# Performance work log

Hardware: AMD Instinct MI355X
Metric: run time of the kernel (lower is better)

Reference implementation:

```python
import jax, jax.numpy as jnp
import numpy as np

# Model dims: H features, N half-state-size, R low-rank, CH output channels, KL kernel length
H, N, R, CH, KL = 512, 64, 1, 1, 4096


def setup_inputs() -> dict:
    key = jax.random.key(0)
    ks = jax.random.split(key, 8)
    log_dt = jax.random.uniform(ks[0], (H,), minval=float(np.log(1e-3)), maxval=float(np.log(1e-1)), dtype=jnp.float32)
    # Hurwitz-like poles: negative real part, HiPPO-like imaginary ladder
    w_re = -0.5 - jax.random.uniform(ks[1], (H, N), dtype=jnp.float32)
    w_im = jnp.broadcast_to(np.float32(np.pi) * jnp.arange(N, dtype=jnp.float32), (H, N))
    B_re = jax.random.normal(ks[2], (1, H, N), dtype=jnp.float32)
    B_im = jax.random.normal(ks[3], (1, H, N), dtype=jnp.float32)
    # small low-rank correction keeps the Woodbury denominator away from zero
    P_re = 0.1 * jax.random.normal(ks[4], (R, H, N), dtype=jnp.float32)
    P_im = 0.1 * jax.random.normal(ks[5], (R, H, N), dtype=jnp.float32)
    C_re = jax.random.normal(ks[6], (CH, H, N), dtype=jnp.float32)
    C_im = jax.random.normal(ks[7], (CH, H, N), dtype=jnp.float32)
    return dict(log_dt=log_dt, w_re=w_re, w_im=w_im, B_re=B_re, B_im=B_im,
                P_re=P_re, P_im=P_im, C_re=C_re, C_im=C_im, L=KL)


def _kernel(log_dt, w_re, w_im, B_re, B_im, P_re, P_im, C_re, C_im, L):
    dt = jnp.exp(log_dt)                                   # (H,)
    w = (w_re + 1j * w_im) * dt[:, None]                   # (H,N) discretized poles w*dt
    B = B_re + 1j * B_im                                   # (1,H,N)
    P = P_re + 1j * P_im                                   # (R,H,N)
    Q = jnp.conj(P)                                        # hurwitz=False path: Q = conj(P)
    C = C_re + 1j * C_im                                   # (CH,H,N)

    Lf = L // 2 + 1
    kk = jnp.arange(Lf)
    omega = jnp.exp((-2j * np.pi) * kk / L)                # FFT roots of unity (complex64)
    den = 1.0 + omega
    # Nyquist node (omega = -1) handled analytically below; guard the division
    safe_den = jnp.where(jnp.abs(den) < 1e-6, jnp.ones_like(den), den)
    z = 2.0 * (1.0 - omega) / safe_den                     # bilinear-transform nodes

    Bc = jnp.concatenate([B, P], axis=0)                   # (1+R,H,N)
    Cc = jnp.concatenate([C, Q], axis=0)                   # (CH+R,H,N)
    v = Bc[:, None] * Cc[None]                             # (1+R,CH+R,H,N)

    # Cauchy kernel: r[a,b,h,l] = sum_n v[a,b,h,n] / (z[l] - w[h,n])
    recip = 1.0 / (z[None, None, :] - w[:, :, None])       # (H,N,Lf)
    r = jnp.einsum('abhn,hnl->abhl', v, recip)             # (1+R,CH+R,H,Lf)
    r = r * dt[None, None, :, None]

    # rank-1 Woodbury correction
    k_f = r[:-1, :-1] - r[:-1, -1:] * r[-1:, :-1] / (1.0 + r[-1:, -1:])
    k_f = k_f * 2.0 / safe_den

    if L % 2 == 0:
        # analytic z -> inf limit at the Nyquist node: dt/2 * sum_n v00
        nyq = 0.5 * dt[None, None, :] * jnp.sum(v[:-1, :-1], axis=-1)  # (1,CH,H)
        k_f = k_f.at[..., -1].set(nyq)

    k = jnp.fft.irfft(k_f, n=L, axis=-1)[..., :L]          # (1,CH,H,L) real
    return k[-1]                                           # (CH,H,L)


def reference(log_dt, w_re, w_im, B_re, B_im, P_re, P_im, C_re, C_im, L):
    return _kernel(log_dt, w_re, w_im, B_re, B_im, P_re, P_im, C_re, C_im, L)
```

## Files before the change

### kernel.cpp

```cpp
#include <hip/hip_runtime.h>
#include <hip/hip_bf16.h>
#include <math.h>


#define HH   512
#define NN   64
#define LLEN 4096
#define MM   2048
#define NTHREADS 512
#define ZPAD(i) ((i) + ((i) >> 4))

typedef float v2f __attribute__((ext_vector_type(2)));

__device__ __forceinline__ float sinr(float r) { return __builtin_amdgcn_sinf(r); }
__device__ __forceinline__ float cosr(float r) { return __builtin_amdgcn_cosf(r); }
__device__ __forceinline__ float rcpf(float x) { return __builtin_amdgcn_rcpf(x); }

__device__ __forceinline__ void cauchy_step(
    const v2f tv, const v2f mwi, const v2f nr, const v2f wr2,
    const v2f v00r, const v2f v00i, const v2f v01r, const v2f v01i,
    const v2f v10r, const v2f v10i, const v2f v11,
    v2f& a00r, v2f& a00i, v2f& a01r, v2f& a01i,
    v2f& a10r, v2f& a10i, v2f& a11r, v2f& a11i)
{
    const v2f dim = __builtin_elementwise_fma(tv, (v2f){2.0f, 2.0f}, mwi);
    const v2f den = __builtin_elementwise_fma(dim, dim, wr2);
    const float ip = rcpf(den.x * den.y);
    v2f inv; inv.x = den.y * ip; inv.y = den.x * ip;
    const v2f ur = nr * inv;
    const v2f ui = -(dim * inv);
    a00r = __builtin_elementwise_fma( v00r, ur, a00r);
    a00r = __builtin_elementwise_fma(-v00i, ui, a00r);
    a00i = __builtin_elementwise_fma( v00r, ui, a00i);
    a00i = __builtin_elementwise_fma( v00i, ur, a00i);
    a01r = __builtin_elementwise_fma( v01r, ur, a01r);
    a01r = __builtin_elementwise_fma(-v01i, ui, a01r);
    a01i = __builtin_elementwise_fma( v01r, ui, a01i);
    a01i = __builtin_elementwise_fma( v01i, ur, a01i);
    a10r = __builtin_elementwise_fma( v10r, ur, a10r);
    a10r = __builtin_elementwise_fma(-v10i, ui, a10r);
    a10i = __builtin_elementwise_fma( v10r, ui, a10i);
    a10i = __builtin_elementwise_fma( v10i, ur, a10i);
    a11r = __builtin_elementwise_fma( v11,  ur, a11r);
    a11i = __builtin_elementwise_fma( v11,  ui, a11i);
}

__device__ __forceinline__ void woodbury_K(
    const v2f tv,
    const v2f a00r, const v2f a00i, const v2f a01r, const v2f a01i,
    const v2f a10r, const v2f a10i, const v2f a11r, const v2f a11i,
    v2f& Kr, v2f& Ki)
{
    const v2f dr = a11r + 1.0f;
    const v2f di = a11i;
    const v2f dd = __builtin_elementwise_fma(dr, dr, di * di);
    v2f dinv; dinv.x = rcpf(dd.x); dinv.y = rcpf(dd.y);
    const v2f numr = a01r * a10r - a01i * a10i;
    const v2f numi = a01r * a10i + a01i * a10r;
    const v2f cr = (numr * dr + numi * di) * dinv;
    const v2f ci = (numi * dr - numr * di) * dinv;
    const v2f Wr = a00r - cr;
    const v2f Wi = a00i - ci;
    Kr = __builtin_elementwise_fma(-tv, Wi, Wr);
    Ki = __builtin_elementwise_fma( tv, Wr, Wi);
}

__global__ __launch_bounds__(NTHREADS, 4) void ssknplr_kernel(
    const float* __restrict__ log_dt,
    const float* __restrict__ w_re, const float* __restrict__ w_im,
    const float* __restrict__ B_re, const float* __restrict__ B_im,
    const float* __restrict__ P_re, const float* __restrict__ P_im,
    const float* __restrict__ C_re, const float* __restrict__ C_im,
    float* __restrict__ out)
{
    __shared__ float4 s_q0[NN];
    __shared__ float4 s_q1[NN];
    __shared__ float2 s_q2[NN];
    __shared__ float2 s_Z[ZPAD(MM) + 1];

    const int h   = blockIdx.x;
    const int tid = threadIdx.x;

    if (tid < NN) {
        const int n   = tid;
        const int idx = h * NN + n;
        const float dt = expf(log_dt[h]);
        const float wr = w_re[idx] * dt;
        const float wi = w_im[idx] * dt;
        const float Br = B_re[idx], Bi = B_im[idx];
        const float Pr = P_re[idx], Pi = P_im[idx];
        const float Cr = C_re[idx], Ci = C_im[idx];
        const float v00r = dt * (Br * Cr - Bi * Ci);
        const float v00i = dt * (Br * Ci + Bi * Cr);
        const float v01r = dt * (Br * Pr + Bi * Pi);
        const float v01i = dt * (Bi * Pr - Br * Pi);
        const float v10r = dt * (Pr * Cr - Pi * Ci);
        const float v10i = dt * (Pr * Ci + Pi * Cr);
        const float v11  = dt * (Pr * Pr + Pi * Pi);
        s_q0[n] = make_float4(-wi, -wr, wr * wr, v00r);
        s_q1[n] = make_float4(v00i, v01r, v01i, v10r);
        s_q2[n] = make_float2(v10i, v11);
    }
    __syncthreads();

    v2f tvA, tvB;
    {
        const float rA = (float)tid         * (1.0f / 8192.0f);
        const float rB = (float)(tid + 512) * (1.0f / 8192.0f);
        const float sA = sinr(rA), cA = cosr(rA);
        const float sB = sinr(rB), cB = cosr(rB);
        tvA.x = sA * rcpf(cA);
        tvA.y = (tid == 0) ? 1.0f : cA * rcpf(sA);
        tvB.x = sB * rcpf(cB);
        tvB.y = cB * rcpf(sB);
    }

    v2f A00r = {0.f,0.f}, A00i = {0.f,0.f}, A01r = {0.f,0.f}, A01i = {0.f,0.f};
    v2f A10r = {0.f,0.f}, A10i = {0.f,0.f}, A11r = {0.f,0.f}, A11i = {0.f,0.f};
    v2f B00r = {0.f,0.f}, B00i = {0.f,0.f}, B01r = {0.f,0.f}, B01i = {0.f,0.f};
    v2f B10r = {0.f,0.f}, B10i = {0.f,0.f}, B11r = {0.f,0.f}, B11i = {0.f,0.f};

    #pragma unroll 4
    for (int n = 0; n < NN; ++n) {
        const float4 q0 = s_q0[n];
        const float4 q1 = s_q1[n];
        const float2 q2 = s_q2[n];
        const v2f mwi  = {q0.x, q0.x}, nr   = {q0.y, q0.y}, wr2 = {q0.z, q0.z};
        const v2f v00r = {q0.w, q0.w}, v00i = {q1.x, q1.x};
        const v2f v01r = {q1.y, q1.y}, v01i = {q1.z, q1.z};
        const v2f v10r = {q1.w, q1.w}, v10i = {q2.x, q2.x};
        const v2f v11  = {q2.y, q2.y};
        cauchy_step(tvA, mwi, nr, wr2, v00r, v00i, v01r, v01i, v10r, v10i, v11,
                    A00r, A00i, A01r, A01i, A10r, A10i, A11r, A11i);
        cauchy_step(tvB, mwi, nr, wr2, v00r, v00i, v01r, v01i, v10r, v10i, v11,
                    B00r, B00i, B01r, B01i, B10r, B10i, B11r, B11i);
    }

    {
        v2f Kr, Ki;
        woodbury_K(tvA, A00r, A00i, A01r, A01i, A10r, A10i, A11r, A11i, Kr, Ki);
        if (tid == 0) {
            float sr = 0.f;
            for (int n = 0; n < NN; ++n) sr += s_q0[n].w;
            const float KN = 0.5f * sr;
            s_Z[ZPAD(0)]    = make_float2(0.5f * (Kr.x + KN), 0.5f * (Kr.x - KN));
            s_Z[ZPAD(1024)] = make_float2(Kr.y, -Ki.y);
        } else {
            const int k = tid, Mk = MM - tid;
            const float rk = (float)k * (1.0f / 4096.0f);
            const float sk = sinr(rk), ck = cosr(rk);
            const float Pr = 0.5f * (Kr.x + Kr.y), Pi = 0.5f * (Ki.x - Ki.y);
            const float Dr = 0.5f * (Kr.x - Kr.y), Di = 0.5f * (Ki.x + Ki.y);
            const float al = sk * Dr + ck * Di;
            const float be = ck * Dr - sk * Di;
            s_Z[ZPAD(k)]  = make_float2(Pr - al, Pi + be);
            s_Z[ZPAD(Mk)] = make_float2(Pr + al, be - Pi);
        }
    }
    {
        v2f Kr, Ki;
        woodbury_K(tvB, B00r, B00i, B01r, B01i, B10r, B10i, B11r, B11i, Kr, Ki);
        const int k = 512 + tid, Mk = 1536 - tid;
        const float rk = (float)k * (1.0f / 4096.0f);
        const float sk = sinr(rk), ck = cosr(rk);
        const float Pr = 0.5f * (Kr.x + Kr.y), Pi = 0.5f * (Ki.x - Ki.y);
        const float Dr = 0.5f * (Kr.x - Kr.y), Di = 0.5f * (Ki.x + Ki.y);
        const float al = sk * Dr + ck * Di;
        const float be = ck * Dr - sk * Di;
        s_Z[ZPAD(k)]  = make_float2(Pr - al, Pi + be);
        s_Z[ZPAD(Mk)] = make_float2(Pr + al, be - Pi);
    }
    __syncthreads();

    for (int s = 10; s >= 1; s -= 2) {
        const int H = 1 << s;
        const int Q = H >> 1;
        const float scale = rcpf((float)(2 * H));
        {
            const int b    = tid;
            const int j    = b & (Q - 1);
            const int base = ((b >> (s - 1)) << (s + 1)) + j;
            const int i0 = base, i1 = base + Q, i2 = base + H, i3 = base + H + Q;
            const float rev = (float)j * scale;
            const float c  = cosr(rev);
            const float sn = sinr(rev);
            const float wbr = c * c - sn * sn;
            const float wbi = 2.0f * c * sn;
            const float2 u0 = s_Z[ZPAD(i0)];
            const float2 u1 = s_Z[ZPAD(i1)];
            const float2 u2 = s_Z[ZPAD(i2)];
            const float2 u3 = s_Z[ZPAD(i3)];
            const float a0r = u0.x + u2.x, a0i = u0.y + u2.y;
            const float d0r = u0.x - u2.x, d0i = u0.y - u2.y;
            const float a1r = u1.x + u3.x, a1i = u1.y + u3.y;
            const float d1r = u1.x - u3.x, d1i = u1.y - u3.y;
            const float e0r = d0r * c  - d0i * sn, e0i = d0r * sn + d0i * c;
            const float e1r = -(d1r * sn) - d1i * c, e1i = d1r * c - d1i * sn;
            s_Z[ZPAD(i0)] = make_float2(a0r + a1r, a0i + a1i);
            const float t0r = a0r - a1r, t0i = a0i - a1i;
            s_Z[ZPAD(i1)] = make_float2(t0r * wbr - t0i * wbi, t0r * wbi + t0i * wbr);
            s_Z[ZPAD(i2)] = make_float2(e0r + e1r, e0i + e1i);
            const float t1r = e0r - e1r, t1i = e0i - e1i;
            s_Z[ZPAD(i3)] = make_float2(t1r * wbr - t1i * wbi, t1r * wbi + t1i * wbr);
        }
        __syncthreads();
    }

    {
        const float scale = 1.0f / (float)MM;
        const int r0 = (int)(__brev((unsigned)tid) >> 21);
        const int zb = ZPAD(r0);
        const float2 z0 = s_Z[zb + 0];
        const float2 z1 = s_Z[zb + 1];
        const float2 z2 = s_Z[zb + 2];
        const float2 z3 = s_Z[zb + 3];
        float2* o2 = (float2*)out + (size_t)h * MM;
        o2[tid]        = make_float2((z0.x + z1.x) * scale, (z0.y + z1.y) * scale);
        o2[tid + 512]  = make_float2((z2.x + z3.x) * scale, (z2.y + z3.y) * scale);
        o2[tid + 1024] = make_float2((z0.x - z1.x) * scale, (z0.y - z1.y) * scale);
        o2[tid + 1536] = make_float2((z2.x - z3.x) * scale, (z2.y - z3.y) * scale);
    }
}

extern "C" void kernel_launch(void* const* d_in, const int* in_sizes, int n_in,
                              void* d_out, int out_size, void* d_ws, size_t ws_size,
                              hipStream_t stream) {
    const float* log_dt = (const float*)d_in[0];
    const float* w_re   = (const float*)d_in[1];
    const float* w_im   = (const float*)d_in[2];
    const float* B_re   = (const float*)d_in[3];
    const float* B_im   = (const float*)d_in[4];
    const float* P_re   = (const float*)d_in[5];
    const float* P_im   = (const float*)d_in[6];
    const float* C_re   = (const float*)d_in[7];
    const float* C_im   = (const float*)d_in[8];
    float* out = (float*)d_out;

    ssknplr_kernel<<<dim3(HH), dim3(NTHREADS), 0, stream>>>(
        log_dt, w_re, w_im, B_re, B_im, P_re, P_im, C_re, C_im, out);
}
```

Before: 35.05 us.

## Halve block size, four Cauchy points per thread, radix-8 inverse FFT

The block shrinks from 512 to 256 threads, and each thread now evaluates four pairs of Cauchy frequency nodes instead of two. The five radix-4 FFT passes, each followed by a barrier, are replaced by three radix-8 passes and a final pair of radix-4 butterflies. The shared-memory padding formula changes to reduce bank conflicts for the new strides. This cuts barrier count and shared-memory round trips. In exchange it raises per-thread register pressure (32 v2f accumulators) and lowers launch_bounds occupancy to 2.

```diff
diff --git a/kernel.cpp b/kernel.cpp
--- a/kernel.cpp
+++ b/kernel.cpp
@@ -7,8 +7,8 @@
 #define NN   64
 #define LLEN 4096
 #define MM   2048
-#define NTHREADS 512
-#define ZPAD(i) ((i) + ((i) >> 4))
+#define NTHREADS 256
+#define ZP(i) ((i) + ((i) >> 4) + ((i) >> 8))
 
 typedef float v2f __attribute__((ext_vector_type(2)));
 
@@ -65,7 +65,57 @@
     Ki = __builtin_elementwise_fma( tv, Wr, Wi);
 }
 
-__global__ __launch_bounds__(NTHREADS, 4) void ssknplr_kernel(
+__device__ __forceinline__ void radix8(float xr[8], float xi[8], const float rev)
+{
+    const float c   = cosr(rev), s = sinr(rev);
+    const float w2r = c * c - s * s, w2i = 2.0f * c * s;
+    const float w4r = w2r * w2r - w2i * w2i;
+    const float w4i = 2.0f * w2r * w2i;
+    const float RH  = 0.70710678118654752440f;
+    const float cms = RH * (c - s), cps = RH * (c + s);
+
+    const float Ar0 = xr[0] + xr[4], Ai0 = xi[0] + xi[4];
+    const float Ar1 = xr[1] + xr[5], Ai1 = xi[1] + xi[5];
+    const float Ar2 = xr[2] + xr[6], Ai2 = xi[2] + xi[6];
+    const float Ar3 = xr[3] + xr[7], Ai3 = xi[3] + xi[7];
+    float dr, di;
+    dr = xr[0] - xr[4]; di = xi[0] - xi[4];
+    const float Br0 = dr * c - di * s,      Bi0 = dr * s + di * c;
+    dr = xr[1] - xr[5]; di = xi[1] - xi[5];
+    const float Br1 = dr * cms - di * cps,  Bi1 = dr * cps + di * cms;
+    dr = xr[2] - xr[6]; di = xi[2] - xi[6];
+    const float Br2 = -dr * s - di * c,     Bi2 = dr * c - di * s;
+    dr = xr[3] - xr[7]; di = xi[3] - xi[7];
+    const float Br3 = -dr * cps - di * cms, Bi3 = dr * cms - di * cps;
+
+    const float Cr0 = Ar0 + Ar2, Ci0 = Ai0 + Ai2;
+    const float Cr1 = Ar1 + Ar3, Ci1 = Ai1 + Ai3;
+    dr = Ar0 - Ar2; di = Ai0 - Ai2;
+    const float Dr0 = dr * w2r - di * w2i,  Di0 = dr * w2i + di * w2r;
+    dr = Ar1 - Ar3; di = Ai1 - Ai3;
+    const float Dr1 = -dr * w2i - di * w2r, Di1 = dr * w2r - di * w2i;
+    const float Er0 = Br0 + Br2, Ei0 = Bi0 + Bi2;
+    const float Er1 = Br1 + Br3, Ei1 = Bi1 + Bi3;
+    dr = Br0 - Br2; di = Bi0 - Bi2;
+    const float Fr0 = dr * w2r - di * w2i,  Fi0 = dr * w2i + di * w2r;
+    dr = Br1 - Br3; di = Bi1 - Bi3;
+    const float Fr1 = -dr * w2i - di * w2r, Fi1 = dr * w2r - di * w2i;
+
+    xr[0] = Cr0 + Cr1; xi[0] = Ci0 + Ci1;
+    dr = Cr0 - Cr1; di = Ci0 - Ci1;
+    xr[1] = dr * w4r - di * w4i; xi[1] = dr * w4i + di * w4r;
+    xr[2] = Dr0 + Dr1; xi[2] = Di0 + Di1;
+    dr = Dr0 - Dr1; di = Di0 - Di1;
+    xr[3] = dr * w4r - di * w4i; xi[3] = dr * w4i + di * w4r;
+    xr[4] = Er0 + Er1; xi[4] = Ei0 + Ei1;
+    dr = Er0 - Er1; di = Ei0 - Ei1;
+    xr[5] = dr * w4r - di * w4i; xi[5] = dr * w4i + di * w4r;
+    xr[6] = Fr0 + Fr1; xi[6] = Fi0 + Fi1;
+    dr = Fr0 - Fr1; di = Fi0 - Fi1;
+    xr[7] = dr * w4r - di * w4i; xi[7] = dr * w4i + di * w4r;
+}
+
+__global__ __launch_bounds__(NTHREADS, 2) void ssknplr_kernel(
     const float* __restrict__ log_dt,
     const float* __restrict__ w_re, const float* __restrict__ w_im,
     const float* __restrict__ B_re, const float* __restrict__ B_im,
@@ -76,7 +126,7 @@
     __shared__ float4 s_q0[NN];
     __shared__ float4 s_q1[NN];
     __shared__ float2 s_q2[NN];
-    __shared__ float2 s_Z[ZPAD(MM) + 1];
+    __shared__ float2 s_Z[ZP(MM - 1) + 1];
 
     const int h   = blockIdx.x;
     const int tid = threadIdx.x;
@@ -103,24 +153,33 @@
     }
     __syncthreads();
 
-    v2f tvA, tvB;
+    v2f tvA, tvB, tvC, tvD;
     {
         const float rA = (float)tid         * (1.0f / 8192.0f);
-        const float rB = (float)(tid + 512) * (1.0f / 8192.0f);
+        const float rB = (float)(tid + 256) * (1.0f / 8192.0f);
+        const float rC = (float)(tid + 512) * (1.0f / 8192.0f);
+        const float rD = (float)(tid + 768) * (1.0f / 8192.0f);
         const float sA = sinr(rA), cA = cosr(rA);
         const float sB = sinr(rB), cB = cosr(rB);
+        const float sC = sinr(rC), cC = cosr(rC);
+        const float sD = sinr(rD), cD = cosr(rD);
         tvA.x = sA * rcpf(cA);
         tvA.y = (tid == 0) ? 1.0f : cA * rcpf(sA);
-        tvB.x = sB * rcpf(cB);
-        tvB.y = cB * rcpf(sB);
-    }
-
-    v2f A00r = {0.f,0.f}, A00i = {0.f,0.f}, A01r = {0.f,0.f}, A01i = {0.f,0.f};
-    v2f A10r = {0.f,0.f}, A10i = {0.f,0.f}, A11r = {0.f,0.f}, A11i = {0.f,0.f};
-    v2f B00r = {0.f,0.f}, B00i = {0.f,0.f}, B01r = {0.f,0.f}, B01i = {0.f,0.f};
-    v2f B10r = {0.f,0.f}, B10i = {0.f,0.f}, B11r = {0.f,0.f}, B11i = {0.f,0.f};
-
-    #pragma unroll 4
+        tvB.x = sB * rcpf(cB);  tvB.y = cB * rcpf(sB);
+        tvC.x = sC * rcpf(cC);  tvC.y = cC * rcpf(sC);
+        tvD.x = sD * rcpf(cD);  tvD.y = cD * rcpf(sD);
+    }
+
+    v2f A00r={0.f,0.f},A00i={0.f,0.f},A01r={0.f,0.f},A01i={0.f,0.f};
+    v2f A10r={0.f,0.f},A10i={0.f,0.f},A11r={0.f,0.f},A11i={0.f,0.f};
+    v2f B00r={0.f,0.f},B00i={0.f,0.f},B01r={0.f,0.f},B01i={0.f,0.f};
+    v2f B10r={0.f,0.f},B10i={0.f,0.f},B11r={0.f,0.f},B11i={0.f,0.f};
+    v2f C00r={0.f,0.f},C00i={0.f,0.f},C01r={0.f,0.f},C01i={0.f,0.f};
+    v2f C10r={0.f,0.f},C10i={0.f,0.f},C11r={0.f,0.f},C11i={0.f,0.f};
+    v2f D00r={0.f,0.f},D00i={0.f,0.f},D01r={0.f,0.f},D01i={0.f,0.f};
+    v2f D10r={0.f,0.f},D10i={0.f,0.f},D11r={0.f,0.f},D11i={0.f,0.f};
+
+    #pragma unroll 2
     for (int n = 0; n < NN; ++n) {
         const float4 q0 = s_q0[n];
         const float4 q1 = s_q1[n];
@@ -134,6 +193,10 @@
                     A00r, A00i, A01r, A01i, A10r, A10i, A11r, A11i);
         cauchy_step(tvB, mwi, nr, wr2, v00r, v00i, v01r, v01i, v10r, v10i, v11,
                     B00r, B00i, B01r, B01i, B10r, B10i, B11r, B11i);
+        cauchy_step(tvC, mwi, nr, wr2, v00r, v00i, v01r, v01i, v10r, v10i, v11,
+                    C00r, C00i, C01r, C01i, C10r, C10i, C11r, C11i);
+        cauchy_step(tvD, mwi, nr, wr2, v00r, v00i, v01r, v01i, v10r, v10i, v11,
+                    D00r, D00i, D01r, D01i, D10r, D10i, D11r, D11i);
     }
 
     {
@@ -143,8 +206,8 @@
             float sr = 0.f;
             for (int n = 0; n < NN; ++n) sr += s_q0[n].w;
             const float KN = 0.5f * sr;
-            s_Z[ZPAD(0)]    = make_float2(0.5f * (Kr.x + KN), 0.5f * (Kr.x - KN));
-            s_Z[ZPAD(1024)] = make_float2(Kr.y, -Ki.y);
+            s_Z[ZP(0)]    = make_float2(0.5f * (Kr.x + KN), 0.5f * (Kr.x - KN));
+            s_Z[ZP(1024)] = make_float2(Kr.y, -Ki.y);
         } else {
             const int k = tid, Mk = MM - tid;
             const float rk = (float)k * (1.0f / 4096.0f);
@@ -153,72 +216,103 @@
             const float Dr = 0.5f * (Kr.x - Kr.y), Di = 0.5f * (Ki.x + Ki.y);
             const float al = sk * Dr + ck * Di;
             const float be = ck * Dr - sk * Di;
-            s_Z[ZPAD(k)]  = make_float2(Pr - al, Pi + be);
-            s_Z[ZPAD(Mk)] = make_float2(Pr + al, be - Pi);
-        }
-    }
-    {
+            s_Z[ZP(k)]  = make_float2(Pr - al, Pi + be);
+            s_Z[ZP(Mk)] = make_float2(Pr + al, be - Pi);
+        }
+    }
+    #pragma unroll
+    for (int c = 1; c < 4; ++c) {
         v2f Kr, Ki;
-        woodbury_K(tvB, B00r, B00i, B01r, B01i, B10r, B10i, B11r, B11i, Kr, Ki);
-        const int k = 512 + tid, Mk = 1536 - tid;
+        if (c == 1) woodbury_K(tvB, B00r,B00i,B01r,B01i,B10r,B10i,B11r,B11i, Kr, Ki);
+        else if (c == 2) woodbury_K(tvC, C00r,C00i,C01r,C01i,C10r,C10i,C11r,C11i, Kr, Ki);
+        else woodbury_K(tvD, D00r,D00i,D01r,D01i,D10r,D10i,D11r,D11i, Kr, Ki);
+        const int k = tid + c * 256, Mk = MM - k;
         const float rk = (float)k * (1.0f / 4096.0f);
         const float sk = sinr(rk), ck = cosr(rk);
         const float Pr = 0.5f * (Kr.x + Kr.y), Pi = 0.5f * (Ki.x - Ki.y);
         const float Dr = 0.5f * (Kr.x - Kr.y), Di = 0.5f * (Ki.x + Ki.y);
         const float al = sk * Dr + ck * Di;
         const float be = ck * Dr - sk * Di;
-        s_Z[ZPAD(k)]  = make_float2(Pr - al, Pi + be);
-        s_Z[ZPAD(Mk)] = make_float2(Pr + al, be - Pi);
-    }
-    __syncthreads();
-
-    for (int s = 10; s >= 1; s -= 2) {
-        const int H = 1 << s;
-        const int Q = H >> 1;
-        const float scale = rcpf((float)(2 * H));
-        {
-            const int b    = tid;
-            const int j    = b & (Q - 1);
-            const int base = ((b >> (s - 1)) << (s + 1)) + j;
-            const int i0 = base, i1 = base + Q, i2 = base + H, i3 = base + H + Q;
-            const float rev = (float)j * scale;
-            const float c  = cosr(rev);
-            const float sn = sinr(rev);
-            const float wbr = c * c - sn * sn;
-            const float wbi = 2.0f * c * sn;
-            const float2 u0 = s_Z[ZPAD(i0)];
-            const float2 u1 = s_Z[ZPAD(i1)];
-            const float2 u2 = s_Z[ZPAD(i2)];
-            const float2 u3 = s_Z[ZPAD(i3)];
-            const float a0r = u0.x + u2.x, a0i = u0.y + u2.y;
-            const float d0r = u0.x - u2.x, d0i = u0.y - u2.y;
-            const float a1r = u1.x + u3.x, a1i = u1.y + u3.y;
-            const float d1r = u1.x - u3.x, d1i = u1.y - u3.y;
-            const float e0r = d0r * c  - d0i * sn, e0i = d0r * sn + d0i * c;
-            const float e1r = -(d1r * sn) - d1i * c, e1i = d1r * c - d1i * sn;
-            s_Z[ZPAD(i0)] = make_float2(a0r + a1r, a0i + a1i);
-            const float t0r = a0r - a1r, t0i = a0i - a1i;
-            s_Z[ZPAD(i1)] = make_float2(t0r * wbr - t0i * wbi, t0r * wbi + t0i * wbr);
-            s_Z[ZPAD(i2)] = make_float2(e0r + e1r, e0i + e1i);
-            const float t1r = e0r - e1r, t1i = e0i - e1i;
-            s_Z[ZPAD(i3)] = make_float2(t1r * wbr - t1i * wbi, t1r * wbi + t1i * wbr);
-        }
-        __syncthreads();
-    }
-
-    {
-        const float scale = 1.0f / (float)MM;
-        const int r0 = (int)(__brev((unsigned)tid) >> 21);
-        const int zb = ZPAD(r0);
-        const float2 z0 = s_Z[zb + 0];
-        const float2 z1 = s_Z[zb + 1];
-        const float2 z2 = s_Z[zb + 2];
-        const float2 z3 = s_Z[zb + 3];
-        float2* o2 = (float2*)out + (size_t)h * MM;
-        o2[tid]        = make_float2((z0.x + z1.x) * scale, (z0.y + z1.y) * scale);
-        o2[tid + 512]  = make_float2((z2.x + z3.x) * scale, (z2.y + z3.y) * scale);
-        o2[tid + 1024] = make_float2((z0.x - z1.x) * scale, (z0.y - z1.y) * scale);
-        o2[tid + 1536] = make_float2((z2.x - z3.x) * scale, (z2.y - z3.y) * scale);
+        s_Z[ZP(k)]  = make_float2(Pr - al, Pi + be);
+        s_Z[ZP(Mk)] = make_float2(Pr + al, be - Pi);
+    }
+    __syncthreads();
+
+    float xr[8], xi[8];
+
+    #pragma unroll
+    for (int q = 0; q < 8; ++q) {
+        const float2 z = s_Z[ZP(tid + (q << 8))];
+        xr[q] = z.x; xi[q] = z.y;
+    }
+    radix8(xr, xi, (float)tid * (1.0f / 2048.0f));
+    #pragma unroll
+    for (int q = 0; q < 8; ++q)
+        s_Z[ZP(tid + (q << 8))] = make_float2(xr[q], xi[q]);
+    __syncthreads();
+
+    {
+        const int base = ((tid >> 5) << 8) + (tid & 31);
+        #pragma unroll
+        for (int q = 0; q < 8; ++q) {
+            const float2 z = s_Z[ZP(base + (q << 5))];
+            xr[q] = z.x; xi[q] = z.y;
+        }
+        radix8(xr, xi, (float)(tid & 31) * (1.0f / 256.0f));
+        #pragma unroll
+        for (int q = 0; q < 8; ++q)
+            s_Z[ZP(base + (q << 5))] = make_float2(xr[q], xi[q]);
+    }
+    __syncthreads();
+
+    {
+        const int base = ((tid >> 2) << 5) + (tid & 3);
+        #pragma unroll
+        for (int q = 0; q < 8; ++q) {
+            const float2 z = s_Z[ZP(base + (q << 2))];
+            xr[q] = z.x; xi[q] = z.y;
+        }
+        radix8(xr, xi, (float)(tid & 3) * (1.0f / 32.0f));
+        #pragma unroll
+        for (int q = 0; q < 8; ++q)
+            s_Z[ZP(base + (q << 2))] = make_float2(xr[q], xi[q]);
+    }
+    __syncthreads();
+
+    {
+        const int i0 = tid << 3;
+        #pragma unroll
+        for (int q = 0; q < 8; ++q) {
+            const float2 z = s_Z[ZP(i0 + q)];
+            xr[q] = z.x; xi[q] = z.y;
+        }
+        #pragma unroll
+        for (int g = 0; g < 2; ++g) {
+            const int o = g * 4;
+            const float A0r = xr[o] + xr[o+2],   A0i = xi[o] + xi[o+2];
+            const float A1r = xr[o+1] + xr[o+3], A1i = xi[o+1] + xi[o+3];
+            const float B0r = xr[o] - xr[o+2],   B0i = xi[o] - xi[o+2];
+            const float B1r = -(xi[o+1] - xi[o+3]);
+            const float B1i =  (xr[o+1] - xr[o+3]);
+            xr[o]   = A0r + A1r; xi[o]   = A0i + A1i;
+            xr[o+1] = A0r - A1r; xi[o+1] = A0i - A1i;
+            xr[o+2] = B0r + B1r; xi[o+2] = B0i + B1i;
+            xr[o+3] = B0r - B1r; xi[o+3] = B0i - B1i;
+        }
+        #pragma unroll
+        for (int q = 0; q < 8; ++q)
+            s_Z[ZP(i0 + q)] = make_float2(xr[q], xi[q]);
+    }
+    __syncthreads();
+
+    const float scale = 1.0f / (float)MM;
+    float2* o2 = (float2*)out + (size_t)h * MM;
+    #pragma unroll
+    for (int q = 0; q < 8; ++q) {
+        const int m = tid + (q << 8);
+        const int r = (int)(__brev((unsigned)m) >> 21);
+        const float2 z = s_Z[ZP(r)];
+        o2[m] = make_float2(z.x * scale, z.y * scale);
     }
 }
 
```

After: 37.01 us. 1.06x slower.
